# Performance work log

Measured on AMD Instinct MI355X. Metric: run time of the kernel, lower is better.

The kernel has to match this reference:

```python
import jax, jax.numpy as jnp
import numpy as np

C = 0.1
CLIP_R = 2.3
N_GENUS = 60
N_SPECIES = 4096
EMB = 64


def _project(x, c=C, clip_r=CLIP_R):
    # HypProjector: feature clipping + expmap0 + projection onto Poincare ball
    sqrt_c = c ** 0.5
    n = jnp.maximum(jnp.linalg.norm(x, axis=-1, keepdims=True), 1e-5)
    x = x * jnp.minimum(1.0, clip_r / n)
    n2 = jnp.maximum(jnp.linalg.norm(x, axis=-1, keepdims=True), 1e-5)
    y = jnp.tanh(sqrt_c * n2) / (sqrt_c * n2) * x
    yn = jnp.maximum(jnp.linalg.norm(y, axis=-1, keepdims=True), 1e-5)
    maxnorm = (1.0 - 1e-3) / sqrt_c
    return jnp.where(yn > maxnorm, y / yn * maxnorm, y)


def _dist_matrix(x, y, c=C):
    # pmath.dist_matrix: 2/sqrt(c) * atanh(sqrt(c) * ||(-x) mobius+ y||) pairwise
    sqrt_c = c ** 0.5
    a = -x  # [N, D]
    dot = a @ y.T                      # [N, M]
    a2 = jnp.sum(a * a, axis=-1)       # [N]
    y2 = jnp.sum(y * y, axis=-1)       # [M]
    coef_a = 1.0 + 2.0 * c * dot + c * y2[None, :]          # [N, M]
    coef_y = 1.0 - c * a2                                    # [N]
    num = coef_a[..., None] * a[:, None, :] + coef_y[:, None, None] * y[None, :, :]  # [N, M, D]
    denom = 1.0 + 2.0 * c * dot + (c * c) * a2[:, None] * y2[None, :]               # [N, M]
    madd_norm = jnp.linalg.norm(num, axis=-1) / jnp.maximum(jnp.abs(denom), 1e-15)
    arg = jnp.clip(sqrt_c * madd_norm, 0.0, 1.0 - 1e-5)
    return (2.0 / sqrt_c) * jnp.arctanh(arg)


def _loss(X, gp_tan, sp_tan, T_species, s2g):
    hyp_g = _project(gp_tan)   # [G, D]
    hyp_s = _project(sp_tan)   # [S, D]
    # species-level proxy-anchor
    D = _dist_matrix(X, hyp_s)                                   # [B, S]
    P = jax.nn.one_hot(T_species, N_SPECIES, dtype=D.dtype)      # [B, S]
    valid_s = (P.sum(0) > 0).astype(D.dtype)
    nvs = jnp.maximum(valid_s.sum(), 1.0)
    loss_sp = (jnp.sum(jax.nn.softplus(D) * P) / nvs
               + jnp.sum(jax.nn.softplus(-D) * (1.0 - P)) / N_SPECIES)
    # genus-level: sum over unique species present in batch (presence mask == unique)
    present = jnp.zeros((N_SPECIES,), D.dtype).at[T_species].set(1.0)  # [S]
    Dg = _dist_matrix(hyp_s, hyp_g)                                     # [S, G]
    oh_g = jax.nn.one_hot(s2g, N_GENUS, dtype=D.dtype)                  # [S, G]
    Pg = oh_g * present[:, None]
    Ng = (1.0 - oh_g) * present[:, None]
    valid_g = (Pg.sum(0) > 0).astype(D.dtype)
    nvg = jnp.maximum(valid_g.sum(), 1.0)
    loss_g = (jnp.sum(jax.nn.softplus(Dg) * Pg) / nvg
              + jnp.sum(jax.nn.softplus(-Dg) * Ng) / N_GENUS)
    return loss_sp + loss_g


def setup_inputs() -> dict:
    key = jax.random.key(0)
    k1, k2, k3, k4, k5, k6 = jax.random.split(key, 6)
    X = jax.random.normal(k1, (1024, EMB), jnp.float32) * 0.05
    T_species = jax.random.randint(k2, (1024,), 0, N_SPECIES)
    T_genus = jax.random.randint(k3, (1024,), 0, N_GENUS)
    s2g = jax.random.randint(k4, (N_SPECIES,), 0, N_GENUS)
    genus_proxies_tan = jax.random.normal(k5, (N_GENUS, EMB), jnp.float32) * 0.01
    species_proxies_tan = jax.random.normal(k6, (N_SPECIES, EMB), jnp.float32) * 0.01
    return {"X": X, "T_species": T_species, "T_genus": T_genus, "s2g": s2g,
            "genus_proxies_tan": genus_proxies_tan, "species_proxies_tan": species_proxies_tan}


def reference(X, T_species, T_genus, s2g, genus_proxies_tan, species_proxies_tan):
    return _loss(X, genus_proxies_tan, species_proxies_tan, T_species, s2g)
```

## Files before the change

kernel.cpp:

```cpp
#include <hip/hip_runtime.h>
#include <math.h>

constexpr float C_CURV = 0.1f;
constexpr float SQRT_C = 0.31622776601683794f;

constexpr int N_GENUS   = 60;
constexpr int N_SPECIES = 4096;
constexpr int NB        = 1024;
constexpr int EMB       = 64;

constexpr int OFF_HYP_S = 0;
constexpr int OFF_HYP_G = OFF_HYP_S + N_SPECIES * EMB;
constexpr int OFF_S2    = OFF_HYP_G + N_GENUS * EMB;
constexpr int OFF_G2    = OFF_S2 + N_SPECIES;
constexpr int OFF_X2    = OFF_G2 + 64;
constexpr int OFF_CNT   = OFF_X2 + NB;
constexpr int OFF_NVG   = OFF_CNT + 1;
constexpr int OFF_SPART = OFF_CNT + 2;
constexpr int OFF_GPART = OFF_SPART + 2 * NB;
constexpr int OFF_LIST  = OFF_GPART + 2 * NB;

__device__ __forceinline__ float wave_sum(float v) {
    #pragma unroll
    for (int off = 32; off; off >>= 1) v += __shfl_xor(v, off);
    return v;
}

__device__ __forceinline__ void pair_terms(float dot_ay, float a2, float y2,
                                           float& d, float& sp_neg) {
    float ca   = fmaf(2.0f * C_CURV, dot_ay, fmaf(C_CURV, y2, 1.0f));
    float cy   = fmaf(-C_CURV, a2, 1.0f);
    float num2 = fmaf(ca * ca, a2, fmaf(2.0f * ca * cy, dot_ay, cy * cy * y2));
    float den  = fmaf(2.0f * C_CURV, dot_ay, fmaf(C_CURV * C_CURV, a2 * y2, 1.0f));
    float arg  = SQRT_C * __builtin_amdgcn_sqrtf(fmaxf(num2, 0.0f))
                        * __builtin_amdgcn_rcpf(fmaxf(fabsf(den), 1e-15f));
    arg = fminf(arg, 1.0f - 1e-5f);
    float u = (1.0f - arg) * __builtin_amdgcn_rcpf(1.0f + arg);
    float L = __builtin_amdgcn_logf(u);
    d       = -2.19201176f * L;
    float e = __builtin_amdgcn_exp2f(3.16227766f * L);
    sp_neg  = 0.69314718f * __builtin_amdgcn_logf(1.0f + e);
}

__global__ __launch_bounds__(256) void k_project(
    const float* __restrict__ X, const float* __restrict__ gp,
    const float* __restrict__ sp, float* __restrict__ ws)
{
    int wave = (blockIdx.x * blockDim.x + threadIdx.x) >> 6;
    int lane = threadIdx.x & 63;
    if (wave >= N_SPECIES + N_GENUS + NB) return;

    float v;
    if (wave < N_SPECIES)                 v = sp[wave * EMB + lane];
    else if (wave < N_SPECIES + N_GENUS)  v = gp[(wave - N_SPECIES) * EMB + lane];
    else                                  v = X[(wave - N_SPECIES - N_GENUS) * EMB + lane];

    float ss = wave_sum(v * v);
    if (wave >= N_SPECIES + N_GENUS) {
        if (lane == 0) ws[OFF_X2 + (wave - N_SPECIES - N_GENUS)] = ss;
        return;
    }

    float n  = fmaxf(sqrtf(ss), 1e-5f);
    v *= fminf(1.0f, 2.3f / n);
    float n2 = fminf(n, 2.3f);
    float fac = tanhf(SQRT_C * n2) / (SQRT_C * n2);
    float y = fac * v;
    float ss2 = wave_sum(y * y);
    float yn = fmaxf(sqrtf(ss2), 1e-5f);
    const float maxnorm = (1.0f - 1e-3f) / SQRT_C;
    if (yn > maxnorm) {
        y *= maxnorm / yn;
        ss2 = wave_sum(y * y);
    }
    if (wave < N_SPECIES) {
        ws[OFF_HYP_S + wave * EMB + lane] = y;
        if (lane == 0) ws[OFF_S2 + wave] = ss2;
    } else {
        int g = wave - N_SPECIES;
        ws[OFF_HYP_G + g * EMB + lane] = y;
        if (lane == 0) ws[OFF_G2 + g] = ss2;
    }
}

__global__ __launch_bounds__(1024) void k_masks(
    const int* __restrict__ Ts, const int* __restrict__ s2g, float* __restrict__ ws)
{
    __shared__ unsigned char pres[N_SPECIES];
    __shared__ unsigned char gm[64];
    __shared__ int scnt, gcnt;
    int t = threadIdx.x;
    int* wsI = (int*)ws;
    for (int s = t; s < N_SPECIES; s += 1024) pres[s] = 0;
    if (t < 64) gm[t] = 0;
    if (t == 0) { scnt = 0; gcnt = 0; }
    __syncthreads();
    pres[Ts[t]] = 1;
    __syncthreads();
    for (int s = t; s < N_SPECIES; s += 1024) {
        if (pres[s]) {
            gm[s2g[s]] = 1;
            int idx = atomicAdd(&scnt, 1);
            wsI[OFF_LIST + idx] = s;
        }
    }
    __syncthreads();
    if (t < N_GENUS && gm[t]) atomicAdd(&gcnt, 1);
    __syncthreads();
    if (t == 0) { wsI[OFF_CNT] = scnt; ws[OFF_NVG] = (float)gcnt; }
}

#define LDPAD 68
__global__ __launch_bounds__(256) void k_species_dist(
    const float* __restrict__ X, const int* __restrict__ Ts, float* __restrict__ ws)
{
    __shared__ float xs[64][LDPAD];
    __shared__ float ssm[64][LDPAD];
    __shared__ float x2s[64], s2s[64];
    __shared__ int   tss[64];
    __shared__ float red[8];

    int t = threadIdx.x;
    int sBase = blockIdx.x * 64;
    int bBase = blockIdx.y * 64;

    #pragma unroll
    for (int r = 0; r < 16; ++r) {
        int flat = r * 256 + t;
        int row = flat >> 6, k = flat & 63;
        xs[row][k]  = X[(bBase + row) * EMB + k];
        ssm[row][k] = ws[OFF_HYP_S + (sBase + row) * EMB + k];
    }
    if (t < 64) {
        x2s[t] = ws[OFF_X2 + bBase + t];
        s2s[t] = ws[OFF_S2 + sBase + t];
        tss[t] = Ts[bBase + t];
    }
    __syncthreads();

    int sx = t & 15, sy = t >> 4;
    float acc[4][4];
    #pragma unroll
    for (int i = 0; i < 4; ++i)
        #pragma unroll
        for (int j = 0; j < 4; ++j) acc[i][j] = 0.0f;

    #pragma unroll
    for (int k = 0; k < EMB; k += 4) {
        float4 av[4], bv[4];
        #pragma unroll
        for (int i = 0; i < 4; ++i)
            av[i] = *reinterpret_cast<const float4*>(&xs[sy + 16 * i][k]);
        #pragma unroll
        for (int j = 0; j < 4; ++j)
            bv[j] = *reinterpret_cast<const float4*>(&ssm[sx + 16 * j][k]);
        #pragma unroll
        for (int i = 0; i < 4; ++i)
            #pragma unroll
            for (int j = 0; j < 4; ++j)
                acc[i][j] = fmaf(av[i].x, bv[j].x, fmaf(av[i].y, bv[j].y,
                            fmaf(av[i].z, bv[j].z, fmaf(av[i].w, bv[j].w, acc[i][j]))));
    }

    float pos = 0.0f, neg = 0.0f;
    #pragma unroll
    for (int i = 0; i < 4; ++i) {
        int bl = sy + 16 * i;
        float a2 = x2s[bl];
        int target = tss[bl];
        #pragma unroll
        for (int j = 0; j < 4; ++j) {
            int sl = sx + 16 * j;
            float d, l;
            pair_terms(-acc[i][j], a2, s2s[sl], d, l);
            if (target == sBase + sl) pos += d + l;
            else                      neg += l;
        }
    }
    pos = wave_sum(pos);
    neg = wave_sum(neg);
    int w = t >> 6;
    if ((t & 63) == 0) { red[2 * w] = pos; red[2 * w + 1] = neg; }
    __syncthreads();
    if (t == 0) {
        float2 out;
        out.x = red[0] + red[2] + red[4] + red[6];
        out.y = red[1] + red[3] + red[5] + red[7];
        int blk = blockIdx.y * gridDim.x + blockIdx.x;
        reinterpret_cast<float2*>(ws + OFF_SPART)[blk] = out;
    }
}

__global__ __launch_bounds__(256) void k_genus_dist(
    const int* __restrict__ s2g, float* __restrict__ ws)
{
    __shared__ float hgt[EMB][61];
    __shared__ float hs[4][EMB];
    __shared__ float g2s[64];

    int t = threadIdx.x;
    const int* wsI = (const int*)ws;
    int cnt  = wsI[OFF_CNT];
    int w    = t >> 6, lane = t & 63;
    int item = blockIdx.x * 4 + w;
    int s    = (item < cnt) ? wsI[OFF_LIST + item] : -1;

    for (int idx = t; idx < N_GENUS * EMB; idx += 256)
        hgt[idx & 63][idx >> 6] = ws[OFF_HYP_G + idx];
    if (t < 64) g2s[t] = (t < N_GENUS) ? ws[OFF_G2 + t] : 0.0f;
    if (s >= 0) hs[w][lane] = ws[OFF_HYP_S + s * EMB + lane];
    __syncthreads();

    float pos = 0.0f, neg = 0.0f;
    if (s >= 0 && lane < N_GENUS) {
        float dot = 0.0f;
        #pragma unroll
        for (int k = 0; k < EMB; ++k) dot = fmaf(hs[w][k], hgt[k][lane], dot);
        float d, l;
        pair_terms(-dot, ws[OFF_S2 + s], g2s[lane], d, l);
        if (s2g[s] == lane) pos = d + l;
        else                neg = l;
    }
    pos = wave_sum(pos);
    neg = wave_sum(neg);
    if (lane == 0) {
        float2 out; out.x = pos; out.y = neg;
        reinterpret_cast<float2*>(ws + OFF_GPART)[item] = out;
    }
}

__global__ __launch_bounds__(256) void k_final(const float* __restrict__ ws, float* __restrict__ out)
{
    __shared__ float red[16];
    int t = threadIdx.x;
    const float2* sp = reinterpret_cast<const float2*>(ws + OFF_SPART);
    const float2* gp = reinterpret_cast<const float2*>(ws + OFF_GPART);
    float ps = 0.0f, ns = 0.0f, pg = 0.0f, ng = 0.0f;
    for (int i = t; i < NB; i += 256) {
        float2 a = sp[i]; ps += a.x; ns += a.y;
        float2 b = gp[i]; pg += b.x; ng += b.y;
    }
    ps = wave_sum(ps); ns = wave_sum(ns); pg = wave_sum(pg); ng = wave_sum(ng);
    int w = t >> 6;
    if ((t & 63) == 0) { red[4*w] = ps; red[4*w+1] = ns; red[4*w+2] = pg; red[4*w+3] = ng; }
    __syncthreads();
    if (t == 0) {
        ps = red[0] + red[4] + red[8]  + red[12];
        ns = red[1] + red[5] + red[9]  + red[13];
        pg = red[2] + red[6] + red[10] + red[14];
        ng = red[3] + red[7] + red[11] + red[15];
        const int* wsI = (const int*)ws;
        float nvs = fmaxf((float)wsI[OFF_CNT], 1.0f);
        float nvg = fmaxf(ws[OFF_NVG], 1.0f);
        out[0] = ps / nvs + ns / (float)N_SPECIES + pg / nvg + ng / (float)N_GENUS;
    }
}

extern "C" void kernel_launch(void* const* d_in, const int* in_sizes, int n_in,
                              void* d_out, int out_size, void* d_ws, size_t ws_size,
                              hipStream_t stream) {
    const float* X   = (const float*)d_in[0];
    const int*   Ts  = (const int*)d_in[1];
    const int*   s2g = (const int*)d_in[3];
    const float* gp  = (const float*)d_in[4];
    const float* sp  = (const float*)d_in[5];
    float* ws  = (float*)d_ws;
    float* out = (float*)d_out;

    k_project<<<(N_SPECIES + N_GENUS + NB) / 4, 256, 0, stream>>>(X, gp, sp, ws);
    k_masks<<<1, 1024, 0, stream>>>(Ts, s2g, ws);
    dim3 g3(N_SPECIES / 64, NB / 64);
    k_species_dist<<<g3, 256, 0, stream>>>(X, Ts, ws);
    k_genus_dist<<<256, 256, 0, stream>>>(s2g, ws);
    k_final<<<1, 256, 0, stream>>>(ws, out);
}
```

Before: 92.71 us.

## Use bf16 MFMA for species distances and merge kernels into prep/dist launches

The projection kernel now also writes bf16 copies of X and the species proxies. The species-distance GEMM switches from fp32 FMA tiles to bf16 16x16x32 MFMA instructions. The mask kernel is folded into the projection launch as an extra block, the genus kernel into the distance launch as extra blocks, and tanh/div are replaced with exp2/rcp intrinsics. This cuts the launch count from five to three and speeds up the dot products, at the cost of bf16 rounding in the dot products feeding atanh distances.

```diff
diff --git a/kernel.cpp b/kernel.cpp
--- a/kernel.cpp
+++ b/kernel.cpp
@@ -19,11 +19,23 @@
 constexpr int OFF_SPART = OFF_CNT + 2;
 constexpr int OFF_GPART = OFF_SPART + 2 * NB;
 constexpr int OFF_LIST  = OFF_GPART + 2 * NB;
+constexpr int OFF_XBF   = ((OFF_LIST + NB + 3) / 4) * 4;
+constexpr int OFF_SBF   = OFF_XBF + NB * 72 / 2;
+constexpr int BFSTRIDE  = 72;
+
+typedef short  bf16x8 __attribute__((ext_vector_type(8)));
+typedef float  f32x4  __attribute__((ext_vector_type(4)));
 
 __device__ __forceinline__ float wave_sum(float v) {
     #pragma unroll
     for (int off = 32; off; off >>= 1) v += __shfl_xor(v, off);
     return v;
+}
+
+__device__ __forceinline__ unsigned short f2bf(float f) {
+    unsigned int u = __builtin_bit_cast(unsigned int, f);
+    u += 0x7FFFu + ((u >> 16) & 1u);
+    return (unsigned short)(u >> 16);
 }
 
 __device__ __forceinline__ void pair_terms(float dot_ay, float a2, float y2,
@@ -42,13 +54,44 @@
     sp_neg  = 0.69314718f * __builtin_amdgcn_logf(1.0f + e);
 }
 
-__global__ __launch_bounds__(256) void k_project(
-    const float* __restrict__ X, const float* __restrict__ gp,
+__global__ __launch_bounds__(256) void k_prep(
+    const float* __restrict__ X, const int* __restrict__ Ts,
+    const int* __restrict__ s2g, const float* __restrict__ gp,
     const float* __restrict__ sp, float* __restrict__ ws)
 {
-    int wave = (blockIdx.x * blockDim.x + threadIdx.x) >> 6;
-    int lane = threadIdx.x & 63;
-    if (wave >= N_SPECIES + N_GENUS + NB) return;
+    __shared__ unsigned char pres[N_SPECIES];
+    __shared__ unsigned char gm[64];
+    __shared__ int scnt, gcnt;
+
+    int t = threadIdx.x;
+    unsigned short* xbf = (unsigned short*)(ws + OFF_XBF);
+    unsigned short* sbf = (unsigned short*)(ws + OFF_SBF);
+
+    if (blockIdx.x == 1295) {
+        int* wsI = (int*)ws;
+        for (int s = t; s < N_SPECIES; s += 256) pres[s] = 0;
+        if (t < 64) gm[t] = 0;
+        if (t == 0) { scnt = 0; gcnt = 0; }
+        __syncthreads();
+        #pragma unroll
+        for (int i = 0; i < 4; ++i) pres[Ts[t + 256 * i]] = 1;
+        __syncthreads();
+        for (int s = t; s < N_SPECIES; s += 256) {
+            if (pres[s]) {
+                gm[s2g[s]] = 1;
+                int idx = atomicAdd(&scnt, 1);
+                wsI[OFF_LIST + idx] = s;
+            }
+        }
+        __syncthreads();
+        if (t < N_GENUS && gm[t]) atomicAdd(&gcnt, 1);
+        __syncthreads();
+        if (t == 0) { wsI[OFF_CNT] = scnt; ws[OFF_NVG] = (float)gcnt; }
+        return;
+    }
+
+    int wave = blockIdx.x * 4 + (t >> 6);
+    int lane = t & 63;
 
     float v;
     if (wave < N_SPECIES)                 v = sp[wave * EMB + lane];
@@ -57,24 +100,30 @@
 
     float ss = wave_sum(v * v);
     if (wave >= N_SPECIES + N_GENUS) {
-        if (lane == 0) ws[OFF_X2 + (wave - N_SPECIES - N_GENUS)] = ss;
+        int row = wave - N_SPECIES - N_GENUS;
+        xbf[row * BFSTRIDE + lane] = f2bf(v);
+        if (lane == 0) ws[OFF_X2 + row] = ss;
         return;
     }
 
-    float n  = fmaxf(sqrtf(ss), 1e-5f);
-    v *= fminf(1.0f, 2.3f / n);
+    float n  = fmaxf(__builtin_amdgcn_sqrtf(ss), 1e-5f);
+    v *= fminf(1.0f, 2.3f * __builtin_amdgcn_rcpf(n));
     float n2 = fminf(n, 2.3f);
-    float fac = tanhf(SQRT_C * n2) / (SQRT_C * n2);
+    float z  = SQRT_C * n2;
+    float ez = __builtin_amdgcn_exp2f(-2.88539008f * z);
+    float th = (1.0f - ez) * __builtin_amdgcn_rcpf(1.0f + ez);
+    float fac = th * __builtin_amdgcn_rcpf(z);
     float y = fac * v;
     float ss2 = wave_sum(y * y);
-    float yn = fmaxf(sqrtf(ss2), 1e-5f);
+    float yn = fmaxf(__builtin_amdgcn_sqrtf(ss2), 1e-5f);
     const float maxnorm = (1.0f - 1e-3f) / SQRT_C;
     if (yn > maxnorm) {
-        y *= maxnorm / yn;
-        ss2 = wave_sum(y * y);
+        y *= maxnorm * __builtin_amdgcn_rcpf(yn);
+        ss2 = maxnorm * maxnorm;
     }
     if (wave < N_SPECIES) {
         ws[OFF_HYP_S + wave * EMB + lane] = y;
+        sbf[wave * BFSTRIDE + lane] = f2bf(y);
         if (lane == 0) ws[OFF_S2 + wave] = ss2;
     } else {
         int g = wave - N_SPECIES;
@@ -83,149 +132,112 @@
     }
 }
 
-__global__ __launch_bounds__(1024) void k_masks(
+union SharedU {
+    struct {
+        uint4 xs[576];
+        uint4 ss[576];
+        float x2s[64], s2s[64];
+        int   tss[64];
+        float red[8];
+    } sp;
+    struct {
+        float hgt[EMB][61];
+        float hs[4][EMB];
+        float g2s[64];
+    } ge;
+};
+
+__global__ __launch_bounds__(256) void k_dist(
     const int* __restrict__ Ts, const int* __restrict__ s2g, float* __restrict__ ws)
 {
-    __shared__ unsigned char pres[N_SPECIES];
-    __shared__ unsigned char gm[64];
-    __shared__ int scnt, gcnt;
+    __shared__ SharedU sh;
     int t = threadIdx.x;
-    int* wsI = (int*)ws;
-    for (int s = t; s < N_SPECIES; s += 1024) pres[s] = 0;
-    if (t < 64) gm[t] = 0;
-    if (t == 0) { scnt = 0; gcnt = 0; }
-    __syncthreads();
-    pres[Ts[t]] = 1;
-    __syncthreads();
-    for (int s = t; s < N_SPECIES; s += 1024) {
-        if (pres[s]) {
-            gm[s2g[s]] = 1;
-            int idx = atomicAdd(&scnt, 1);
-            wsI[OFF_LIST + idx] = s;
-        }
-    }
-    __syncthreads();
-    if (t < N_GENUS && gm[t]) atomicAdd(&gcnt, 1);
-    __syncthreads();
-    if (t == 0) { wsI[OFF_CNT] = scnt; ws[OFF_NVG] = (float)gcnt; }
-}
-
-#define LDPAD 68
-__global__ __launch_bounds__(256) void k_species_dist(
-    const float* __restrict__ X, const int* __restrict__ Ts, float* __restrict__ ws)
-{
-    __shared__ float xs[64][LDPAD];
-    __shared__ float ssm[64][LDPAD];
-    __shared__ float x2s[64], s2s[64];
-    __shared__ int   tss[64];
-    __shared__ float red[8];
-
-    int t = threadIdx.x;
-    int sBase = blockIdx.x * 64;
-    int bBase = blockIdx.y * 64;
-
-    #pragma unroll
-    for (int r = 0; r < 16; ++r) {
-        int flat = r * 256 + t;
-        int row = flat >> 6, k = flat & 63;
-        xs[row][k]  = X[(bBase + row) * EMB + k];
-        ssm[row][k] = ws[OFF_HYP_S + (sBase + row) * EMB + k];
-    }
-    if (t < 64) {
-        x2s[t] = ws[OFF_X2 + bBase + t];
-        s2s[t] = ws[OFF_S2 + sBase + t];
-        tss[t] = Ts[bBase + t];
-    }
-    __syncthreads();
-
-    int sx = t & 15, sy = t >> 4;
-    float acc[4][4];
-    #pragma unroll
-    for (int i = 0; i < 4; ++i)
+    int bx = blockIdx.x;
+
+    if (bx < 1024) {
+        int sBase = (bx & 63) * 64;
+        int bBase = (bx >> 6) * 64;
+        const unsigned short* xbf = (const unsigned short*)(ws + OFF_XBF);
+        const unsigned short* sbf = (const unsigned short*)(ws + OFF_SBF);
+        const uint4* srcx = (const uint4*)(xbf + bBase * BFSTRIDE);
+        const uint4* srcs = (const uint4*)(sbf + sBase * BFSTRIDE);
+        for (int i = t; i < 576; i += 256) { sh.sp.xs[i] = srcx[i]; sh.sp.ss[i] = srcs[i]; }
+        if (t < 64) {
+            sh.sp.x2s[t] = ws[OFF_X2 + bBase + t];
+            sh.sp.s2s[t] = ws[OFF_S2 + sBase + t];
+            sh.sp.tss[t] = Ts[bBase + t];
+        }
+        __syncthreads();
+
+        int lane = t & 63, w = t >> 6;
+        int nloc = lane & 15, quad = lane >> 4;
+        const unsigned short* xs = (const unsigned short*)sh.sp.xs;
+        const unsigned short* sb = (const unsigned short*)sh.sp.ss;
+
+        f32x4 acc[4] = {{0.f,0.f,0.f,0.f},{0.f,0.f,0.f,0.f},{0.f,0.f,0.f,0.f},{0.f,0.f,0.f,0.f}};
         #pragma unroll
-        for (int j = 0; j < 4; ++j) acc[i][j] = 0.0f;
-
-    #pragma unroll
-    for (int k = 0; k < EMB; k += 4) {
-        float4 av[4], bv[4];
+        for (int k0 = 0; k0 < EMB; k0 += 32) {
+            bf16x8 a = *(const bf16x8*)(xs + (16 * w + nloc) * BFSTRIDE + k0 + quad * 8);
+            #pragma unroll
+            for (int jt = 0; jt < 4; ++jt) {
+                bf16x8 b = *(const bf16x8*)(sb + (16 * jt + nloc) * BFSTRIDE + k0 + quad * 8);
+                acc[jt] = __builtin_amdgcn_mfma_f32_16x16x32_bf16(a, b, acc[jt], 0, 0, 0);
+            }
+        }
+
+        float pos = 0.0f, neg = 0.0f;
         #pragma unroll
-        for (int i = 0; i < 4; ++i)
-            av[i] = *reinterpret_cast<const float4*>(&xs[sy + 16 * i][k]);
-        #pragma unroll
-        for (int j = 0; j < 4; ++j)
-            bv[j] = *reinterpret_cast<const float4*>(&ssm[sx + 16 * j][k]);
-        #pragma unroll
-        for (int i = 0; i < 4; ++i)
+        for (int jt = 0; jt < 4; ++jt) {
+            int sl = 16 * jt + nloc;
+            float y2 = sh.sp.s2s[sl];
             #pragma unroll
-            for (int j = 0; j < 4; ++j)
-                acc[i][j] = fmaf(av[i].x, bv[j].x, fmaf(av[i].y, bv[j].y,
-                            fmaf(av[i].z, bv[j].z, fmaf(av[i].w, bv[j].w, acc[i][j]))));
-    }
-
-    float pos = 0.0f, neg = 0.0f;
-    #pragma unroll
-    for (int i = 0; i < 4; ++i) {
-        int bl = sy + 16 * i;
-        float a2 = x2s[bl];
-        int target = tss[bl];
-        #pragma unroll
-        for (int j = 0; j < 4; ++j) {
-            int sl = sx + 16 * j;
-            float d, l;
-            pair_terms(-acc[i][j], a2, s2s[sl], d, l);
-            if (target == sBase + sl) pos += d + l;
-            else                      neg += l;
-        }
-    }
-    pos = wave_sum(pos);
-    neg = wave_sum(neg);
-    int w = t >> 6;
-    if ((t & 63) == 0) { red[2 * w] = pos; red[2 * w + 1] = neg; }
-    __syncthreads();
-    if (t == 0) {
-        float2 out;
-        out.x = red[0] + red[2] + red[4] + red[6];
-        out.y = red[1] + red[3] + red[5] + red[7];
-        int blk = blockIdx.y * gridDim.x + blockIdx.x;
-        reinterpret_cast<float2*>(ws + OFF_SPART)[blk] = out;
-    }
-}
-
-__global__ __launch_bounds__(256) void k_genus_dist(
-    const int* __restrict__ s2g, float* __restrict__ ws)
-{
-    __shared__ float hgt[EMB][61];
-    __shared__ float hs[4][EMB];
-    __shared__ float g2s[64];
-
-    int t = threadIdx.x;
-    const int* wsI = (const int*)ws;
-    int cnt  = wsI[OFF_CNT];
-    int w    = t >> 6, lane = t & 63;
-    int item = blockIdx.x * 4 + w;
-    int s    = (item < cnt) ? wsI[OFF_LIST + item] : -1;
-
-    for (int idx = t; idx < N_GENUS * EMB; idx += 256)
-        hgt[idx & 63][idx >> 6] = ws[OFF_HYP_G + idx];
-    if (t < 64) g2s[t] = (t < N_GENUS) ? ws[OFF_G2 + t] : 0.0f;
-    if (s >= 0) hs[w][lane] = ws[OFF_HYP_S + s * EMB + lane];
-    __syncthreads();
-
-    float pos = 0.0f, neg = 0.0f;
-    if (s >= 0 && lane < N_GENUS) {
-        float dot = 0.0f;
-        #pragma unroll
-        for (int k = 0; k < EMB; ++k) dot = fmaf(hs[w][k], hgt[k][lane], dot);
-        float d, l;
-        pair_terms(-dot, ws[OFF_S2 + s], g2s[lane], d, l);
-        if (s2g[s] == lane) pos = d + l;
-        else                neg = l;
-    }
-    pos = wave_sum(pos);
-    neg = wave_sum(neg);
-    if (lane == 0) {
-        float2 out; out.x = pos; out.y = neg;
-        reinterpret_cast<float2*>(ws + OFF_GPART)[item] = out;
+            for (int r = 0; r < 4; ++r) {
+                int m = 16 * w + quad * 4 + r;
+                float d, lterm;
+                pair_terms(-acc[jt][r], sh.sp.x2s[m], y2, d, lterm);
+                if (sh.sp.tss[m] == sBase + sl) pos += d + lterm;
+                else                            neg += lterm;
+            }
+        }
+        pos = wave_sum(pos);
+        neg = wave_sum(neg);
+        if (lane == 0) { sh.sp.red[2 * w] = pos; sh.sp.red[2 * w + 1] = neg; }
+        __syncthreads();
+        if (t == 0) {
+            float2 o;
+            o.x = sh.sp.red[0] + sh.sp.red[2] + sh.sp.red[4] + sh.sp.red[6];
+            o.y = sh.sp.red[1] + sh.sp.red[3] + sh.sp.red[5] + sh.sp.red[7];
+            reinterpret_cast<float2*>(ws + OFF_SPART)[bx] = o;
+        }
+    } else {
+        const int* wsI = (const int*)ws;
+        int cnt  = wsI[OFF_CNT];
+        int w    = t >> 6, lane = t & 63;
+        int item = (bx - 1024) * 4 + w;
+        int s    = (item < cnt) ? wsI[OFF_LIST + item] : -1;
+
+        for (int idx = t; idx < N_GENUS * EMB; idx += 256)
+            sh.ge.hgt[idx & 63][idx >> 6] = ws[OFF_HYP_G + idx];
+        if (t < 64) sh.ge.g2s[t] = (t < N_GENUS) ? ws[OFF_G2 + t] : 0.0f;
+        if (s >= 0) sh.ge.hs[w][lane] = ws[OFF_HYP_S + s * EMB + lane];
+        __syncthreads();
+
+        float pos = 0.0f, neg = 0.0f;
+        if (s >= 0 && lane < N_GENUS) {
+            float dot = 0.0f;
+            #pragma unroll
+            for (int k = 0; k < EMB; ++k) dot = fmaf(sh.ge.hs[w][k], sh.ge.hgt[k][lane], dot);
+            float d, lterm;
+            pair_terms(-dot, ws[OFF_S2 + s], sh.ge.g2s[lane], d, lterm);
+            if (s2g[s] == lane) pos = d + lterm;
+            else                neg = lterm;
+        }
+        pos = wave_sum(pos);
+        neg = wave_sum(neg);
+        if (lane == 0) {
+            float2 o; o.x = pos; o.y = neg;
+            reinterpret_cast<float2*>(ws + OFF_GPART)[item] = o;
+        }
     }
 }
 
@@ -233,12 +245,12 @@
 {
     __shared__ float red[16];
     int t = threadIdx.x;
-    const float2* sp = reinterpret_cast<const float2*>(ws + OFF_SPART);
-    const float2* gp = reinterpret_cast<const float2*>(ws + OFF_GPART);
+    const float2* spp = reinterpret_cast<const float2*>(ws + OFF_SPART);
+    const float2* gpp = reinterpret_cast<const float2*>(ws + OFF_GPART);
     float ps = 0.0f, ns = 0.0f, pg = 0.0f, ng = 0.0f;
     for (int i = t; i < NB; i += 256) {
-        float2 a = sp[i]; ps += a.x; ns += a.y;
-        float2 b = gp[i]; pg += b.x; ng += b.y;
+        float2 a = spp[i]; ps += a.x; ns += a.y;
+        float2 b = gpp[i]; pg += b.x; ng += b.y;
     }
     ps = wave_sum(ps); ns = wave_sum(ns); pg = wave_sum(pg); ng = wave_sum(ng);
     int w = t >> 6;
@@ -267,10 +279,7 @@
     float* ws  = (float*)d_ws;
     float* out = (float*)d_out;
 
-    k_project<<<(N_SPECIES + N_GENUS + NB) / 4, 256, 0, stream>>>(X, gp, sp, ws);
-    k_masks<<<1, 1024, 0, stream>>>(Ts, s2g, ws);
-    dim3 g3(N_SPECIES / 64, NB / 64);
-    k_species_dist<<<g3, 256, 0, stream>>>(X, Ts, ws);
-    k_genus_dist<<<256, 256, 0, stream>>>(s2g, ws);
+    k_prep<<<1296, 256, 0, stream>>>(X, Ts, s2g, gp, sp, ws);
+    k_dist<<<1280, 256, 0, stream>>>(Ts, s2g, ws);
     k_final<<<1, 256, 0, stream>>>(ws, out);
 }
```

New measurement: 81.97 us. -11.6%, faster.
